# Kernel tuning notes

Hardware: AMD Instinct MI355X
Metric: run time of the kernel (lower is better)

The kernel has to match this reference:

```python
import jax, jax.numpy as jnp
import numpy as np

V = 32000   # vocab_size
L = 4       # n_layer
H = 12      # n_head
C = 768     # n_embd
T = 1024    # block_size / seq len
B = 4       # batch
D = C // H  # head_dim
F = 4 * C   # mlp hidden


def setup_inputs() -> dict:
    key = jax.random.key(0)
    ks = jax.random.split(key, 12)
    n = lambda k, sh: (jax.random.normal(k, sh, dtype=jnp.float32) * 0.02)
    return {
        "idx": jax.random.randint(ks[0], (B, T), 0, V, dtype=jnp.int32),
        "tok_emb": n(ks[1], (V, C)),
        "pos_emb": n(ks[2], (T, C)),
        "Wq": n(ks[3], (L, C, C)),
        "Wk": n(ks[4], (L, C, C)),
        "Wv": n(ks[5], (L, C, C)),
        "Wp": n(ks[6], (L, C, C)),
        "bp": jnp.zeros((L, C), jnp.float32),
        "ln1s": jnp.ones((L, C), jnp.float32),
        "ln1b": jnp.zeros((L, C), jnp.float32),
        "ln2s": jnp.ones((L, C), jnp.float32),
        "ln2b": jnp.zeros((L, C), jnp.float32),
        "W1": n(ks[7], (L, C, F)),
        "b1": jnp.zeros((L, F), jnp.float32),
        "W2": n(ks[8], (L, F, C)),
        "b2": jnp.zeros((L, C), jnp.float32),
        "lnfs": jnp.ones((C,), jnp.float32),
        "lnfb": jnp.zeros((C,), jnp.float32),
        "Whead": n(ks[9], (C, V)),
    }


def _ln(x, s, b):
    m = x.mean(-1, keepdims=True)
    v = ((x - m) ** 2).mean(-1, keepdims=True)
    return (x - m) * jax.lax.rsqrt(v + 1e-5) * s + b


def reference(idx, tok_emb, pos_emb, Wq, Wk, Wv, Wp, bp, ln1s, ln1b, ln2s, ln2b,
              W1, b1, W2, b2, lnfs, lnfb, Whead):
    Bc, Tc = idx.shape
    x = tok_emb[idx] + pos_emb[None, :Tc]               # [B,T,C]
    mask = jnp.tril(jnp.ones((Tc, Tc), bool))           # causal mask
    scale = 1.0 / np.sqrt(D)
    for l in range(L):
        # --- causal self-attention (explicit QK^T, masked softmax) ---
        h = _ln(x, ln1s[l], ln1b[l])
        q = (h @ Wq[l]).reshape(Bc, Tc, H, D).transpose(0, 2, 1, 3)  # [B,H,T,D]
        k = (h @ Wk[l]).reshape(Bc, Tc, H, D).transpose(0, 2, 1, 3)
        v = (h @ Wv[l]).reshape(Bc, Tc, H, D).transpose(0, 2, 1, 3)
        att = jnp.einsum('bhqd,bhkd->bhqk', q, k) * scale            # [B,H,T,T]
        att = jnp.where(mask, att, -jnp.inf)
        att = jax.nn.softmax(att, axis=-1)
        y = jnp.einsum('bhqk,bhkd->bhqd', att, v)
        y = y.transpose(0, 2, 1, 3).reshape(Bc, Tc, C)
        x = x + (y @ Wp[l] + bp[l])
        # --- GELU MLP ---
        h = _ln(x, ln2s[l], ln2b[l])
        x = x + (jax.nn.gelu(h @ W1[l] + b1[l], approximate=False) @ W2[l] + b2[l])
    x = _ln(x, lnfs, lnfb)
    logits = x @ Whead                                  # [B,T,V]
    return logits
```

## Files before the change

kernel.cpp:

```cpp
#include <hip/hip_runtime.h>
#include <stdint.h>

#define B_ 4
#define T_ 1024
#define C_ 768
#define H_ 12
#define D_ 64
#define F_ 3072
#define V_ 32000
#define L_ 4

typedef unsigned short ushort_t;
typedef __bf16 bf16x8 __attribute__((ext_vector_type(8)));
typedef float f32x4 __attribute__((ext_vector_type(4)));
typedef unsigned short u16x8 __attribute__((ext_vector_type(8)));

__device__ __forceinline__ float b2f(unsigned short u) {
    union { unsigned int i; float f; } x; x.i = ((unsigned int)u) << 16; return x.f;
}
__device__ __forceinline__ unsigned short f2b(float f) {
    union { float f; unsigned int i; } x; x.f = f;
    unsigned int r = x.i + 0x7FFFu + ((x.i >> 16) & 1u);
    return (unsigned short)(r >> 16);
}

__device__ __forceinline__ float gelu_f(float u) {
    float z = fabsf(u) * 0.70710678118654752f;
    float t = __builtin_amdgcn_rcpf(1.0f + 0.3275911f * z);
    float poly = t * (0.254829592f + t * (-0.284496736f + t * (1.421413741f +
                 t * (-1.453152027f + t * 1.061405429f))));
    float erfz = 1.0f - poly * __expf(-z * z);
    return u * 0.5f * (1.0f + copysignf(erfz, u));
}

__device__ __forceinline__ void gload16(const ushort_t* g, ushort_t* l) {
    __builtin_amdgcn_global_load_lds(
        (const __attribute__((address_space(1))) unsigned int*)g,
        (__attribute__((address_space(3))) unsigned int*)l, 16, 0, 0);
}

__global__ __launch_bounds__(256) void k_embed(const int* __restrict__ idx,
        const float* __restrict__ tok, const float* __restrict__ pos,
        ushort_t* __restrict__ x) {
    int i = blockIdx.x * 256 + threadIdx.x;
    int m = i / (C_ / 4);
    int cc = (i % (C_ / 4)) * 4;
    int t = m & (T_ - 1);
    int tokid = idx[m];
    float4 te = *(const float4*)&tok[(size_t)tokid * C_ + cc];
    float4 pe = *(const float4*)&pos[(size_t)t * C_ + cc];
    ushort4 o;
    o.x = f2b(te.x + pe.x); o.y = f2b(te.y + pe.y);
    o.z = f2b(te.z + pe.z); o.w = f2b(te.w + pe.w);
    *(ushort4*)&x[(size_t)m * C_ + cc] = o;
}

__global__ __launch_bounds__(256) void k_ln(const ushort_t* __restrict__ x,
        const float* __restrict__ s, const float* __restrict__ b,
        ushort_t* __restrict__ out) {
    const int lane = threadIdx.x & 63, wave = threadIdx.x >> 6;
    const int row = blockIdx.x * 4 + wave;
    const ushort_t* xr = x + (size_t)row * C_;
    float vf[3][4];
    float sum = 0.f, sq = 0.f;
#pragma unroll
    for (int j = 0; j < 3; ++j) {
        ushort4 u = *(const ushort4*)&xr[lane * 4 + j * 256];
        vf[j][0] = b2f(u.x); vf[j][1] = b2f(u.y); vf[j][2] = b2f(u.z); vf[j][3] = b2f(u.w);
#pragma unroll
        for (int e = 0; e < 4; ++e) { sum += vf[j][e]; sq += vf[j][e] * vf[j][e]; }
    }
#pragma unroll
    for (int off = 1; off < 64; off <<= 1) {
        sum += __shfl_xor(sum, off);
        sq  += __shfl_xor(sq,  off);
    }
    float mean = sum * (1.f / C_);
    float var  = sq * (1.f / C_) - mean * mean;
    float rstd = rsqrtf(var + 1e-5f);
#pragma unroll
    for (int j = 0; j < 3; ++j) {
        int c = lane * 4 + j * 256;
        float4 sv = *(const float4*)&s[c];
        float4 bv = *(const float4*)&b[c];
        ushort4 o;
        o.x = f2b((vf[j][0] - mean) * rstd * sv.x + bv.x);
        o.y = f2b((vf[j][1] - mean) * rstd * sv.y + bv.y);
        o.z = f2b((vf[j][2] - mean) * rstd * sv.z + bv.z);
        o.w = f2b((vf[j][3] - mean) * rstd * sv.w + bv.w);
        *(ushort4*)&out[(size_t)row * C_ + c] = o;
    }
}

__global__ void k_tcvt(const float* __restrict__ in, ushort_t* __restrict__ out,
                       int R, int C) {
    __shared__ float tile[32][33];
    const float* src = in + (size_t)blockIdx.z * R * C;
    ushort_t* dst = out + (size_t)blockIdx.z * R * C;
    int r0 = blockIdx.y * 32, c0 = blockIdx.x * 32;
    int tx = threadIdx.x, ty = threadIdx.y;
#pragma unroll
    for (int i = ty; i < 32; i += 8)
        tile[i][tx] = src[(size_t)(r0 + i) * C + c0 + tx];
    __syncthreads();
#pragma unroll
    for (int i = ty; i < 32; i += 8)
        dst[(size_t)(c0 + i) * R + r0 + tx] = f2b(tile[tx][i]);
}

__global__ void k_tcvt16(const float* __restrict__ wq, const float* __restrict__ wk,
                         const float* __restrict__ wv, const float* __restrict__ wp,
                         ushort_t* __restrict__ out) {
    __shared__ float tile[32][33];
    int l = blockIdx.z >> 2, w = blockIdx.z & 3;
    const float* src = (w == 0 ? wq : w == 1 ? wk : w == 2 ? wv : wp) + (size_t)l * C_ * C_;
    ushort_t* dst = out + (size_t)blockIdx.z * C_ * C_;
    int r0 = blockIdx.y * 32, c0 = blockIdx.x * 32;
    int tx = threadIdx.x, ty = threadIdx.y;
#pragma unroll
    for (int i = ty; i < 32; i += 8)
        tile[i][tx] = src[(size_t)(r0 + i) * C_ + c0 + tx];
    __syncthreads();
#pragma unroll
    for (int i = ty; i < 32; i += 8)
        dst[(size_t)(c0 + i) * C_ + r0 + tx] = f2b(tile[tx][i]);
}

template <int EPI>
__global__ __launch_bounds__(256) void k_gemm(
        const ushort_t* __restrict__ A, const ushort_t* __restrict__ BT,
        const float* __restrict__ bias, const float* __restrict__ resid,
        float* __restrict__ outf, ushort_t* __restrict__ outb,
        ushort_t* __restrict__ outb2, ushort_t* __restrict__ outb3,
        int M, int N, int K) {
    __shared__ __align__(16) ushort_t S[24576];
    const int tid = threadIdx.x;
    const int lane = tid & 63, wave = tid >> 6;
    const int lr = lane & 15, lg = lane >> 4;
    const int wm = (wave >> 1) * 64, wn = (wave & 1) * 64;

    const int bid = blockIdx.x;
    const int m_in = bid & 7;
    const int strip = (bid >> 3) & 3;
    const int ncol = bid >> 5;
    const int m0 = (strip * 8 + m_in) << 7;
    const int n0 = ncol << 7;

    const int sr = wave * 16 + (lane >> 2);
    const int sc = (((lane & 3) ^ ((lane >> 3) & 3)) << 3);

    f32x4 acc[4][4];
#pragma unroll
    for (int i = 0; i < 4; ++i)
#pragma unroll
        for (int j = 0; j < 4; ++j) acc[i][j] = (f32x4){0.f, 0.f, 0.f, 0.f};

    auto stage = [&](int k0, int buf) {
        ushort_t* as = S + buf * 4096;
        ushort_t* bs = S + 12288 + buf * 4096;
        gload16(&A [(size_t)(m0 + sr)      * K + k0 + sc], as + (wave * 16) * 32);
        gload16(&A [(size_t)(m0 + 64 + sr) * K + k0 + sc], as + (64 + wave * 16) * 32);
        gload16(&BT[(size_t)(n0 + sr)      * K + k0 + sc], bs + (wave * 16) * 32);
        gload16(&BT[(size_t)(n0 + 64 + sr) * K + k0 + sc], bs + (64 + wave * 16) * 32);
    };

    const int nt = K >> 5;
    stage(0, 0);
    stage(32, 1);
    int cur = 0, pre = 2;
    const int swzr = (lr >> 1) & 3;
    for (int t = 0; t < nt; ++t) {
        if (t + 1 < nt) asm volatile("s_waitcnt vmcnt(4)" ::: "memory");
        else            asm volatile("s_waitcnt vmcnt(0)" ::: "memory");
        __builtin_amdgcn_sched_barrier(0);
        __builtin_amdgcn_s_barrier();
        const ushort_t* as = S + cur * 4096;
        const ushort_t* bs = S + 12288 + cur * 4096;
        bf16x8 af[4], bfr[4];
#pragma unroll
        for (int i = 0; i < 4; ++i)
            af[i]  = *(const bf16x8*)&as[(wm + i * 16 + lr) * 32 + ((lg ^ swzr) << 3)];
#pragma unroll
        for (int j = 0; j < 4; ++j)
            bfr[j] = *(const bf16x8*)&bs[(wn + j * 16 + lr) * 32 + ((lg ^ swzr) << 3)];
        if (t + 2 < nt) stage((t + 2) << 5, pre);
#pragma unroll
        for (int i = 0; i < 4; ++i)
#pragma unroll
            for (int j = 0; j < 4; ++j)
                acc[i][j] = __builtin_amdgcn_mfma_f32_16x16x32_bf16(af[i], bfr[j], acc[i][j], 0, 0, 0);
        cur = (cur == 2) ? 0 : cur + 1;
        pre = (pre == 2) ? 0 : pre + 1;
    }

    if (EPI == 0) {
        float* cls = (float*)S;
#pragma unroll
        for (int h = 0; h < 2; ++h) {
            __syncthreads();
            if ((wm >> 6) == h) {
#pragma unroll
                for (int i = 0; i < 4; ++i)
#pragma unroll
                    for (int j = 0; j < 4; ++j)
#pragma unroll
                        for (int r = 0; r < 4; ++r)
                            cls[(i * 16 + lg * 4 + r) * 128 + wn + j * 16 + lr] = acc[i][j][r];
            }
            __syncthreads();
#pragma unroll
            for (int p = 0; p < 8; ++p) {
                int row = p * 8 + (tid >> 5);
                int colc = (tid & 31) * 4;
                f32x4 val = *(const f32x4*)&cls[row * 128 + colc];
                size_t gidx = (size_t)(m0 + h * 64 + row) * N + n0 + colc;
                __builtin_nontemporal_store(val, (f32x4*)&outf[gidx]);
            }
        }
        return;
    }

    if (EPI == 2) {
        float* cls = (float*)S;
#pragma unroll
        for (int h = 0; h < 2; ++h) {
            __syncthreads();
            if ((wm >> 6) == h) {
#pragma unroll
                for (int i = 0; i < 4; ++i)
#pragma unroll
                    for (int j = 0; j < 4; ++j)
#pragma unroll
                        for (int r = 0; r < 4; ++r)
                            cls[(i * 16 + lg * 4 + r) * 128 + wn + j * 16 + lr] = acc[i][j][r];
            }
            __syncthreads();
#pragma unroll
            for (int p = 0; p < 4; ++p) {
                int idx = p * 256 + tid;
                int row = idx >> 4;
                int colc = (idx & 15) * 8;
                f32x4 v0 = *(const f32x4*)&cls[row * 128 + colc];
                f32x4 v1 = *(const f32x4*)&cls[row * 128 + colc + 4];
                size_t gidx = (size_t)(m0 + h * 64 + row) * N + n0 + colc;
                u16x8 rv = *(const u16x8*)&outb2[gidx];
                f32x4 b0 = *(const f32x4*)&bias[n0 + colc];
                f32x4 b1 = *(const f32x4*)&bias[n0 + colc + 4];
                u16x8 o;
#pragma unroll
                for (int e = 0; e < 4; ++e) o[e]     = f2b(v0[e] + b0[e] + b2f(rv[e]));
#pragma unroll
                for (int e = 0; e < 4; ++e) o[4 + e] = f2b(v1[e] + b1[e] + b2f(rv[4 + e]));
                *(u16x8*)&outb[gidx] = o;
            }
        }
        return;
    }

    if (EPI == 1) {
        ushort_t* cls = S;
        __syncthreads();
#pragma unroll
        for (int i = 0; i < 4; ++i)
#pragma unroll
            for (int j = 0; j < 4; ++j) {
                float bval = bias[n0 + wn + j * 16 + lr];
#pragma unroll
                for (int r = 0; r < 4; ++r)
                    cls[(wm + i * 16 + lg * 4 + r) * 128 + wn + j * 16 + lr] =
                        f2b(gelu_f(acc[i][j][r] + bval));
            }
        __syncthreads();
#pragma unroll
        for (int p = 0; p < 8; ++p) {
            int row = p * 16 + (tid >> 4);
            int colc = (tid & 15) * 8;
            u16x8 val = *(const u16x8*)&cls[row * 128 + colc];
            *(u16x8*)&outb[(size_t)(m0 + row) * N + n0 + colc] = val;
        }
        return;
    }

#pragma unroll
    for (int i = 0; i < 4; ++i) {
#pragma unroll
        for (int j = 0; j < 4; ++j) {
            int col = n0 + wn + j * 16 + lr;
#pragma unroll
            for (int r = 0; r < 4; ++r) {
                int row = m0 + wm + i * 16 + lg * 4 + r;
                float v = acc[i][j][r];
                int nm = col / 768, c = col % 768;
                int hh = c >> 6, d = c & 63;
                int bb = row >> 10, t = row & 1023;
                ushort_t val = f2b(v);
                if (nm == 0)
                    outb [((((size_t)bb * H_ + hh) << 10) + t) * D_ + d] = val;
                else if (nm == 1)
                    outb2[((((size_t)bb * H_ + hh) << 10) + t) * D_ + d] = val;
                else
                    outb3[(((size_t)bb * H_ + hh) * D_ + d) * T_ + t] = val;
            }
        }
    }
}

__global__ __launch_bounds__(256) void k_attn(const ushort_t* __restrict__ q,
        const ushort_t* __restrict__ k, const ushort_t* __restrict__ vT,
        ushort_t* __restrict__ yc) {
    __shared__ __align__(16) ushort_t P[4][16 * 136];
    const int lane = threadIdx.x & 63, wave = threadIdx.x >> 6;
    const int lr = lane & 15, lg = lane >> 4;
    const int bh = blockIdx.x;
    const int bb = bh / H_, hh = bh % H_;
    const int qrow0 = (gridDim.y - 1 - blockIdx.y) * 64 + wave * 16;
    const ushort_t* qb = q + (size_t)bh * T_ * D_;
    const ushort_t* kb = k + (size_t)bh * T_ * D_;
    const ushort_t* vb = vT + (size_t)bh * D_ * T_;

    bf16x8 aq0 = *(const bf16x8*)&qb[(qrow0 + lr) * D_ + lg * 8];
    bf16x8 aq1 = *(const bf16x8*)&qb[(qrow0 + lr) * D_ + 32 + lg * 8];

    f32x4 accY[4];
    float ls = 0.f;
#pragma unroll
    for (int d = 0; d < 4; ++d) accY[d] = (f32x4){0.f, 0.f, 0.f, 0.f};

    ushort_t* pw = &P[wave][0];
    const int kv_end = qrow0 + 16;
    for (int kv0 = 0; kv0 < kv_end; kv0 += 128) {
        const bool full = (kv0 + 127 <= qrow0);
        float p[8][4];
        float ps = 0.f;
#pragma unroll
        for (int j = 0; j < 8; ++j) {
            f32x4 s = (f32x4){0.f, 0.f, 0.f, 0.f};
            bf16x8 bk0 = *(const bf16x8*)&kb[(kv0 + j * 16 + lr) * D_ + lg * 8];
            bf16x8 bk1 = *(const bf16x8*)&kb[(kv0 + j * 16 + lr) * D_ + 32 + lg * 8];
            __builtin_amdgcn_s_setprio(1);
            s = __builtin_amdgcn_mfma_f32_16x16x32_bf16(bk0, aq0, s, 0, 0, 0);
            s = __builtin_amdgcn_mfma_f32_16x16x32_bf16(bk1, aq1, s, 0, 0, 0);
            __builtin_amdgcn_s_setprio(0);
            if (full) {
#pragma unroll
                for (int r = 0; r < 4; ++r) { p[j][r] = __expf(s[r] * 0.125f); ps += p[j][r]; }
            } else {
                int kcb = kv0 + j * 16 + lg * 4;
#pragma unroll
                for (int r = 0; r < 4; ++r) {
                    p[j][r] = (kcb + r <= qrow0 + lr) ? __expf(s[r] * 0.125f) : 0.f;
                    ps += p[j][r];
                }
            }
        }
        ps += __shfl_xor(ps, 16);
        ps += __shfl_xor(ps, 32);
        ls += ps;

        asm volatile("s_waitcnt lgkmcnt(0)" ::: "memory");
        __builtin_amdgcn_sched_barrier(0);
#pragma unroll
        for (int j = 0; j < 8; ++j) {
            unsigned int w0, w1;
            asm("v_cvt_pk_bf16_f32 %0, %1, %2" : "=v"(w0) : "v"(p[j][0]), "v"(p[j][1]));
            asm("v_cvt_pk_bf16_f32 %0, %1, %2" : "=v"(w1) : "v"(p[j][2]), "v"(p[j][3]));
            uint2 w; w.x = w0; w.y = w1;
            *(uint2*)&pw[lr * 136 + j * 16 + lg * 4] = w;
        }
        asm volatile("s_waitcnt lgkmcnt(0)" ::: "memory");
        __builtin_amdgcn_sched_barrier(0);
        bf16x8 pa[4];
#pragma unroll
        for (int ks = 0; ks < 4; ++ks)
            pa[ks] = *(const bf16x8*)&pw[lr * 136 + ks * 32 + lg * 8];
#pragma unroll
        for (int d = 0; d < 4; ++d) {
            __builtin_amdgcn_s_setprio(1);
#pragma unroll
            for (int ks = 0; ks < 4; ++ks) {
                bf16x8 bv = *(const bf16x8*)&vb[(d * 16 + lr) * T_ + kv0 + ks * 32 + lg * 8];
                accY[d] = __builtin_amdgcn_mfma_f32_16x16x32_bf16(pa[ks], bv, accY[d], 0, 0, 0);
            }
            __builtin_amdgcn_s_setprio(0);
        }
    }
    float inv[4];
#pragma unroll
    for (int r = 0; r < 4; ++r) inv[r] = 1.0f / __shfl(ls, lg * 4 + r);
#pragma unroll
    for (int d = 0; d < 4; ++d)
#pragma unroll
        for (int r = 0; r < 4; ++r) {
            int row = qrow0 + lg * 4 + r;
            yc[((size_t)bb * T_ + row) * C_ + hh * D_ + d * 16 + lr] = f2b(accY[d][r] * inv[r]);
        }
}

extern "C" void kernel_launch(void* const* d_in, const int* in_sizes, int n_in,
                              void* d_out, int out_size, void* d_ws, size_t ws_size,
                              hipStream_t stream) {
    (void)in_sizes; (void)n_in; (void)out_size; (void)ws_size;
    const int*   idx  = (const int*)d_in[0];
    const float* tok  = (const float*)d_in[1];
    const float* pos  = (const float*)d_in[2];
    const float* Wq   = (const float*)d_in[3];
    const float* Wk   = (const float*)d_in[4];
    const float* Wv   = (const float*)d_in[5];
    const float* Wp   = (const float*)d_in[6];
    const float* bp   = (const float*)d_in[7];
    const float* ln1s = (const float*)d_in[8];
    const float* ln1b = (const float*)d_in[9];
    const float* ln2s = (const float*)d_in[10];
    const float* ln2b = (const float*)d_in[11];
    const float* W1   = (const float*)d_in[12];
    const float* b1   = (const float*)d_in[13];
    const float* W2   = (const float*)d_in[14];
    const float* b2   = (const float*)d_in[15];
    const float* lnfs = (const float*)d_in[16];
    const float* lnfb = (const float*)d_in[17];
    const float* Wh   = (const float*)d_in[18];
    float* out = (float*)d_out;

    char* ws = (char*)d_ws;
    size_t off = 0;
    auto alloc = [&](size_t bytes) { void* p = ws + off; off += (bytes + 255) & ~(size_t)255; return p; };

    const size_t CCE = (size_t)C_ * C_;
    const size_t CFE = (size_t)C_ * F_;
    ushort_t* wCC  = (ushort_t*)alloc(16 * CCE * 2);
    ushort_t* w1T  = (ushort_t*)alloc((size_t)L_ * CFE * 2);
    ushort_t* w2T  = (ushort_t*)alloc((size_t)L_ * CFE * 2);
    ushort_t* whT  = (ushort_t*)alloc((size_t)C_ * V_ * 2);
    ushort_t* x    = (ushort_t*)alloc((size_t)B_ * T_ * C_ * 2);
    ushort_t* h    = (ushort_t*)alloc((size_t)B_ * T_ * C_ * 2);
    ushort_t* qb_  = (ushort_t*)alloc((size_t)B_ * T_ * C_ * 2);
    ushort_t* kb_  = (ushort_t*)alloc((size_t)B_ * T_ * C_ * 2);
    ushort_t* vTb  = (ushort_t*)alloc((size_t)B_ * T_ * C_ * 2);
    ushort_t* yc   = (ushort_t*)alloc((size_t)B_ * T_ * C_ * 2);
    ushort_t* mh   = (ushort_t*)alloc((size_t)B_ * T_ * F_ * 2);

    dim3 tb(32, 8);
    k_tcvt16<<<dim3(24, 24, 16), tb, 0, stream>>>(Wq, Wk, Wv, Wp, wCC);
    k_tcvt<<<dim3(96, 24, 4), tb, 0, stream>>>(W1, w1T, C_, F_);
    k_tcvt<<<dim3(24, 96, 4), tb, 0, stream>>>(W2, w2T, F_, C_);
    k_tcvt<<<dim3(1000, 24, 1), tb, 0, stream>>>(Wh, whT, C_, V_);

    k_embed<<<3072, 256, 0, stream>>>(idx, tok, pos, x);

    for (int l = 0; l < L_; ++l) {
        k_ln<<<1024, 256, 0, stream>>>(x, ln1s + l * C_, ln1b + l * C_, h);
        k_gemm<3><<<18 * 32, 256, 0, stream>>>(h, wCC + (size_t)(l * 4) * CCE,
            nullptr, nullptr, nullptr, qb_, kb_, vTb, 4096, 3 * C_, C_);
        k_attn<<<dim3(48, 16), 256, 0, stream>>>(qb_, kb_, vTb, yc);
        k_gemm<2><<<6 * 32, 256, 0, stream>>>(yc, wCC + (size_t)(l * 4 + 3) * CCE,
            bp + l * C_, nullptr, nullptr, x, x, nullptr, 4096, C_, C_);
        k_ln<<<1024, 256, 0, stream>>>(x, ln2s + l * C_, ln2b + l * C_, h);
        k_gemm<1><<<24 * 32, 256, 0, stream>>>(h, w1T + (size_t)l * CFE,
            b1 + l * F_, nullptr, nullptr, mh, nullptr, nullptr, 4096, F_, C_);
        k_gemm<2><<<6 * 32, 256, 0, stream>>>(mh, w2T + (size_t)l * CFE,
            b2 + l * C_, nullptr, nullptr, x, x, nullptr, 4096, C_, F_);
    }
    k_ln<<<1024, 256, 0, stream>>>(x, lnfs, lnfb, h);
    k_gemm<0><<<250 * 32, 256, 0, stream>>>(h, whT, nullptr, nullptr,
        out, nullptr, nullptr, nullptr, 4096, V_, C_);
}
```

Baseline: 1.084 ms.

## Add dedicated 128x256-tile head GEMM kernel with 512 threads for logits

```diff
diff --git a/kernel.cpp b/kernel.cpp
--- a/kernel.cpp
+++ b/kernel.cpp
@@ -193,33 +193,6 @@
         pre = (pre == 2) ? 0 : pre + 1;
     }
 
-    if (EPI == 0) {
-        float* cls = (float*)S;
-#pragma unroll
-        for (int h = 0; h < 2; ++h) {
-            __syncthreads();
-            if ((wm >> 6) == h) {
-#pragma unroll
-                for (int i = 0; i < 4; ++i)
-#pragma unroll
-                    for (int j = 0; j < 4; ++j)
-#pragma unroll
-                        for (int r = 0; r < 4; ++r)
-                            cls[(i * 16 + lg * 4 + r) * 128 + wn + j * 16 + lr] = acc[i][j][r];
-            }
-            __syncthreads();
-#pragma unroll
-            for (int p = 0; p < 8; ++p) {
-                int row = p * 8 + (tid >> 5);
-                int colc = (tid & 31) * 4;
-                f32x4 val = *(const f32x4*)&cls[row * 128 + colc];
-                size_t gidx = (size_t)(m0 + h * 64 + row) * N + n0 + colc;
-                __builtin_nontemporal_store(val, (f32x4*)&outf[gidx]);
-            }
-        }
-        return;
-    }
-
     if (EPI == 2) {
         float* cls = (float*)S;
 #pragma unroll
@@ -301,6 +274,94 @@
                 else
                     outb3[(((size_t)bb * H_ + hh) * D_ + d) * T_ + t] = val;
             }
+        }
+    }
+}
+
+__global__ __launch_bounds__(512, 4) void k_gemmh(
+        const ushort_t* __restrict__ A, const ushort_t* __restrict__ BT,
+        float* __restrict__ outf, int M, int N, int K) {
+    __shared__ __align__(16) ushort_t S[36864];
+    const int tid = threadIdx.x;
+    const int lane = tid & 63, wave = tid >> 6;
+    const int lr = lane & 15, lg = lane >> 4;
+    const int wm = (wave >> 2) * 64, wn = (wave & 3) * 64;
+
+    const int bid = blockIdx.x;
+    const int m_in = bid & 7;
+    const int strip = (bid >> 3) & 3;
+    const int ncol = bid >> 5;
+    const int m0 = (strip * 8 + m_in) << 7;
+    const int n0 = ncol << 8;
+
+    const int srr = lane >> 2;
+    const int sc = (((lane & 3) ^ ((lane >> 3) & 3)) << 3);
+
+    f32x4 acc[4][4];
+#pragma unroll
+    for (int i = 0; i < 4; ++i)
+#pragma unroll
+        for (int j = 0; j < 4; ++j) acc[i][j] = (f32x4){0.f, 0.f, 0.f, 0.f};
+
+    auto stage = [&](int k0, int buf) {
+        ushort_t* as = S + buf * 4096;
+        ushort_t* bs = S + 12288 + buf * 8192;
+        gload16(&A [(size_t)(m0 + wave * 16 + srr) * K + k0 + sc], as + (wave * 16) * 32);
+        gload16(&BT[(size_t)(n0 + wave * 32 + srr)      * K + k0 + sc], bs + (wave * 32) * 32);
+        gload16(&BT[(size_t)(n0 + wave * 32 + 16 + srr) * K + k0 + sc], bs + (wave * 32 + 16) * 32);
+    };
+
+    const int nt = K >> 5;
+    stage(0, 0);
+    stage(32, 1);
+    int cur = 0, pre = 2;
+    const int swzr = (lr >> 1) & 3;
+    for (int t = 0; t < nt; ++t) {
+        if (t + 1 < nt) asm volatile("s_waitcnt vmcnt(3)" ::: "memory");
+        else            asm volatile("s_waitcnt vmcnt(0)" ::: "memory");
+        __builtin_amdgcn_sched_barrier(0);
+        __builtin_amdgcn_s_barrier();
+        const ushort_t* as = S + cur * 4096;
+        const ushort_t* bs = S + 12288 + cur * 8192;
+        bf16x8 af[4], bfr[4];
+#pragma unroll
+        for (int i = 0; i < 4; ++i)
+            af[i]  = *(const bf16x8*)&as[(wm + i * 16 + lr) * 32 + ((lg ^ swzr) << 3)];
+#pragma unroll
+        for (int j = 0; j < 4; ++j)
+            bfr[j] = *(const bf16x8*)&bs[(wn + j * 16 + lr) * 32 + ((lg ^ swzr) << 3)];
+        if (t + 2 < nt) stage((t + 2) << 5, pre);
+#pragma unroll
+        for (int i = 0; i < 4; ++i)
+#pragma unroll
+            for (int j = 0; j < 4; ++j)
+                acc[i][j] = __builtin_amdgcn_mfma_f32_16x16x32_bf16(af[i], bfr[j], acc[i][j], 0, 0, 0);
+        cur = (cur == 2) ? 0 : cur + 1;
+        pre = (pre == 2) ? 0 : pre + 1;
+    }
+
+    float* cls = (float*)S;
+#pragma unroll
+    for (int h = 0; h < 2; ++h) {
+        __syncthreads();
+        if ((wm >> 6) == h) {
+#pragma unroll
+            for (int i = 0; i < 4; ++i)
+#pragma unroll
+                for (int j = 0; j < 4; ++j)
+#pragma unroll
+                    for (int r = 0; r < 4; ++r)
+                        cls[(i * 16 + lg * 4 + r) * 260 + wn + j * 16 + lr] = acc[i][j][r];
+        }
+        __syncthreads();
+#pragma unroll
+        for (int p = 0; p < 8; ++p) {
+            int idx = p * 512 + tid;
+            int row = idx >> 6;
+            int colc = (idx & 63) * 4;
+            f32x4 val = *(const f32x4*)&cls[row * 260 + colc];
+            __builtin_nontemporal_store(val,
+                (f32x4*)&outf[(size_t)(m0 + h * 64 + row) * N + n0 + colc]);
         }
     }
 }
@@ -461,6 +522,5 @@
             b2 + l * C_, nullptr, nullptr, x, x, nullptr, 4096, C_, F_);
     }
     k_ln<<<1024, 256, 0, stream>>>(x, lnfs, lnfb, h);
-    k_gemm<0><<<250 * 32, 256, 0, stream>>>(h, whT, nullptr, nullptr,
-        out, nullptr, nullptr, nullptr, 4096, V_, C_);
-}
+    k_gemmh<<<4000, 512, 0, stream>>>(h, whT, out, 4096, V_, C_);
+}
```

Result: no change. 1.065 ms (-1.8%).
